# Kernel optimization log

Measured on AMD Instinct MI355X. Metric: run time of the kernel, lower is better.

The kernel has to match this reference:

```python
import jax, jax.numpy as jnp
import numpy as np

FPS, MS = 7, 256
WIDTHS = [(FPS, 12), (12, 12), (12, 12), (12, 12), (12, 12), (12, 6), (6, 1)]


def setup_inputs() -> dict:
    key = jax.random.key(0)
    keys = jax.random.split(key, 1 + 2 * len(WIDTHS))
    B = 32768
    inp = {"inputs": jax.random.normal(keys[0], (B, MS, FPS), dtype=jnp.float32)}
    for li, (fan_in, fan_out) in enumerate(WIDTHS):
        scale = 1.0 / np.sqrt(fan_in)
        inp[f"W{li}"] = jax.random.uniform(keys[1 + 2 * li], (fan_in, fan_out), dtype=jnp.float32, minval=-scale, maxval=scale)
        inp[f"b{li}"] = jnp.zeros((fan_out,), dtype=jnp.float32)
    return inp


def _mlp(x, Ws, bs):
    # layer 0: linear activation
    h = x @ Ws[0] + bs[0]
    # layers 1-4: relu
    for li in range(1, 5):
        h = jax.nn.relu(h @ Ws[li] + bs[li])
    # layer 5: linear (6 units), layer 6: final linear (1 unit)
    h = h @ Ws[5] + bs[5]
    h = h @ Ws[6] + bs[6]
    return h


def reference(inputs, W0, b0, W1, b1, W2, b2, W3, b3, W4, b4, W5, b5, W6, b6):
    B = inputs.shape[0]
    Ws = [W0, W1, W2, W3, W4, W5, W6]
    bs = [b0, b1, b2, b3, b4, b5, b6]
    # Equivalent to looping over ms slices with the shared MLP then concatenating:
    # fold the ms dim into the batch, run once, reshape back to [B, ms].
    x = inputs.reshape(B * MS, FPS)
    out = _mlp(x, Ws, bs)  # [B*MS, 1]
    return out.reshape(B, MS)
```

## Files before the change

kernel.cpp:

```cpp
#include <hip/hip_runtime.h>

#define R 4
#define NTHREADS 256


__global__ __launch_bounds__(NTHREADS, 4) void mlp_kernel(
    const float* __restrict__ in,
    const float* __restrict__ W0, const float* __restrict__ b0,
    const float* __restrict__ W1, const float* __restrict__ b1,
    const float* __restrict__ W2, const float* __restrict__ b2,
    const float* __restrict__ W3, const float* __restrict__ b3,
    const float* __restrict__ W4, const float* __restrict__ b4,
    const float* __restrict__ W5, const float* __restrict__ b5,
    const float* __restrict__ W6, const float* __restrict__ b6,
    float* __restrict__ out, int nrows)
{
    __shared__ __align__(16) float lds[768];
    const int tid = threadIdx.x;

#define STAGE(off, src, count) \
    for (int k = tid; k < (count); k += NTHREADS) lds[(off) + k] = (src)[k];
    STAGE(0,   W0, 84)  STAGE(96,  b0, 12)
    STAGE(112, W1, 144) STAGE(256, b1, 12)
    STAGE(272, W2, 144) STAGE(416, b2, 12)
    STAGE(432, W3, 144) STAGE(576, b3, 12)
    STAGE(592, W4, 144) STAGE(736, b4, 12)
#undef STAGE
    if (tid < 12) {
        float acc = 0.0f;
        for (int c = 0; c < 6; ++c) acc = fmaf(W5[tid * 6 + c], W6[c], acc);
        lds[752 + tid] = acc;
    } else if (tid == 12) {
        float acc = b6[0];
        for (int c = 0; c < 6; ++c) acc = fmaf(b5[c], W6[c], acc);
        lds[764] = acc;
    }
    __syncthreads();

    const long t = (long)blockIdx.x * NTHREADS + tid;
    const long row0 = t * R;
    if (row0 >= nrows) return;
    const bool full = (row0 + R) <= nrows;

    float xs[28];
    if (full) {
        const float4* ip = (const float4*)(in + row0 * 7);
        float4 q;
        q = ip[0]; xs[0]=q.x;  xs[1]=q.y;  xs[2]=q.z;  xs[3]=q.w;
        q = ip[1]; xs[4]=q.x;  xs[5]=q.y;  xs[6]=q.z;  xs[7]=q.w;
        q = ip[2]; xs[8]=q.x;  xs[9]=q.y;  xs[10]=q.z; xs[11]=q.w;
        q = ip[3]; xs[12]=q.x; xs[13]=q.y; xs[14]=q.z; xs[15]=q.w;
        q = ip[4]; xs[16]=q.x; xs[17]=q.y; xs[18]=q.z; xs[19]=q.w;
        q = ip[5]; xs[20]=q.x; xs[21]=q.y; xs[22]=q.z; xs[23]=q.w;
        q = ip[6]; xs[24]=q.x; xs[25]=q.y; xs[26]=q.z; xs[27]=q.w;
    } else {
        #pragma unroll
        for (int r = 0; r < R; ++r)
            #pragma unroll
            for (int i = 0; i < 7; ++i)
                xs[r * 7 + i] = ((row0 + r) < nrows) ? in[(row0 + r) * 7 + i] : 0.0f;
    }

#define LOADW12(dst, baseptr) { \
    const float4* _p = (const float4*)(baseptr); \
    float4 _a = _p[0], _b = _p[1], _c = _p[2]; \
    dst[0]=_a.x; dst[1]=_a.y; dst[2]=_a.z;  dst[3]=_a.w; \
    dst[4]=_b.x; dst[5]=_b.y; dst[6]=_b.z;  dst[7]=_b.w; \
    dst[8]=_c.x; dst[9]=_c.y; dst[10]=_c.z; dst[11]=_c.w; }

    float h[R][12];

    {
        float bb[12]; LOADW12(bb, lds + 96);
        float w[12];  LOADW12(w, lds + 0);
        #pragma unroll
        for (int r = 0; r < R; ++r)
            #pragma unroll
            for (int j = 0; j < 12; ++j)
                h[r][j] = fmaf(xs[r * 7 + 0], w[j], bb[j]);
        #pragma unroll
        for (int i = 1; i < 7; ++i) {
            LOADW12(w, lds + i * 12);
            #pragma unroll
            for (int r = 0; r < R; ++r)
                #pragma unroll
                for (int j = 0; j < 12; ++j)
                    h[r][j] = fmaf(xs[r * 7 + i], w[j], h[r][j]);
        }
    }

    constexpr int WOFF[4] = {112, 272, 432, 592};
    constexpr int BOFF[4] = {256, 416, 576, 736};
    #pragma unroll
    for (int li = 0; li < 4; ++li) {
        float nxt[R][12];
        {
            float bb[12]; LOADW12(bb, lds + BOFF[li]);
            float w[12];  LOADW12(w, lds + WOFF[li]);
            #pragma unroll
            for (int r = 0; r < R; ++r)
                #pragma unroll
                for (int j = 0; j < 12; ++j)
                    nxt[r][j] = fmaf(h[r][0], w[j], bb[j]);
        }
        #pragma unroll
        for (int i = 1; i < 12; ++i) {
            float w[12]; LOADW12(w, lds + WOFF[li] + i * 12);
            #pragma unroll
            for (int r = 0; r < R; ++r)
                #pragma unroll
                for (int j = 0; j < 12; ++j)
                    nxt[r][j] = fmaf(h[r][i], w[j], nxt[r][j]);
        }
        #pragma unroll
        for (int r = 0; r < R; ++r)
            #pragma unroll
            for (int j = 0; j < 12; ++j)
                h[r][j] = fmaxf(nxt[r][j], 0.0f);
    }

    float w56[12]; LOADW12(w56, lds + 752);
    const float b56 = lds[764];
    float o[R];
    #pragma unroll
    for (int r = 0; r < R; ++r) {
        float acc = fmaf(h[r][0], w56[0], b56);
        #pragma unroll
        for (int i = 1; i < 12; ++i) acc = fmaf(h[r][i], w56[i], acc);
        o[r] = acc;
    }

    if (full) {
        *((float4*)(out + row0)) = make_float4(o[0], o[1], o[2], o[3]);
    } else {
        #pragma unroll
        for (int r = 0; r < R; ++r)
            if ((row0 + r) < nrows) out[row0 + r] = o[r];
    }
#undef LOADW12
}

extern "C" void kernel_launch(void* const* d_in, const int* in_sizes, int n_in,
                              void* d_out, int out_size, void* d_ws, size_t ws_size,
                              hipStream_t stream) {
    const float* in = (const float*)d_in[0];
    const float* W0 = (const float*)d_in[1];  const float* b0 = (const float*)d_in[2];
    const float* W1 = (const float*)d_in[3];  const float* b1 = (const float*)d_in[4];
    const float* W2 = (const float*)d_in[5];  const float* b2 = (const float*)d_in[6];
    const float* W3 = (const float*)d_in[7];  const float* b3 = (const float*)d_in[8];
    const float* W4 = (const float*)d_in[9];  const float* b4 = (const float*)d_in[10];
    const float* W5 = (const float*)d_in[11]; const float* b5 = (const float*)d_in[12];
    const float* W6 = (const float*)d_in[13]; const float* b6 = (const float*)d_in[14];
    float* out = (float*)d_out;

    const int nrows = in_sizes[0] / 7;
    const long nthreads_total = ((long)nrows + R - 1) / R;
    const int blocks = (int)((nthreads_total + NTHREADS - 1) / NTHREADS);

    hipLaunchKernelGGL(mlp_kernel, dim3(blocks), dim3(NTHREADS), 0, stream,
                       in, W0, b0, W1, b1, W2, b2, W3, b3, W4, b4, W5, b5, W6, b6,
                       out, nrows);
}
```

Measured before the change: 128.3 us.

## Run MLP layers on fp16 MFMA with split-precision weights and persistent waves

Replaces the per-thread FP32 FMA MLP with a wave-level MFMA 16x16x32 f16 pipeline. Weights and activations are split into hi/lo fp16 pairs to keep near-FP32 accuracy, and biases are folded in through a constant-one input column. A small pre-kernel builds the weight fragments in the workspace. The main kernel is a grid-stride persistent loop over 16-row tiles with the next tile's input prefetched. This targets the ALU-bound FMA cost, at the price of an extra launch, packing and conversion overhead, and possible precision loss. Rows in a partial last tile (nrows not a multiple of 16) are never computed.

Result: slower. 168.7 us (+31.5%).

```diff
diff --git a/kernel.cpp b/kernel.cpp
--- a/kernel.cpp
+++ b/kernel.cpp
@@ -1,143 +1,148 @@
 #include <hip/hip_runtime.h>
+#include <stdint.h>
 
-#define R 4
-#define NTHREADS 256
+typedef _Float16 half8  __attribute__((ext_vector_type(8)));
+typedef __fp16   fp16x2 __attribute__((ext_vector_type(2)));
+typedef float    floatx4 __attribute__((ext_vector_type(4)));
+typedef uint32_t u32x4  __attribute__((ext_vector_type(4)));
+typedef float    f4a    __attribute__((ext_vector_type(4), aligned(4)));
 
+union FragU { u32x4 v; uint32_t u[4]; half8 h; };
+union H2U   { fp16x2 h; uint32_t u; };
 
-__global__ __launch_bounds__(NTHREADS, 4) void mlp_kernel(
-    const float* __restrict__ in,
-    const float* __restrict__ W0, const float* __restrict__ b0,
-    const float* __restrict__ W1, const float* __restrict__ b1,
-    const float* __restrict__ W2, const float* __restrict__ b2,
-    const float* __restrict__ W3, const float* __restrict__ b3,
-    const float* __restrict__ W4, const float* __restrict__ b4,
-    const float* __restrict__ W5, const float* __restrict__ b5,
-    const float* __restrict__ W6, const float* __restrict__ b6,
-    float* __restrict__ out, int nrows)
+#define NT 256
+#define NBLOCKS 2048
+
+__global__ void build_frags(const float* __restrict__ W0, const float* __restrict__ b0,
+                            const float* __restrict__ W1, const float* __restrict__ b1,
+                            const float* __restrict__ W2, const float* __restrict__ b2,
+                            const float* __restrict__ W3, const float* __restrict__ b3,
+                            const float* __restrict__ W4, const float* __restrict__ b4,
+                            const float* __restrict__ W5, const float* __restrict__ b5,
+                            const float* __restrict__ W6, const float* __restrict__ b6,
+                            uint32_t* __restrict__ ws)
 {
-    __shared__ __align__(16) float lds[768];
-    const int tid = threadIdx.x;
+    const int l = threadIdx.x;
+    if (l >= 64) return;
+    const int m = l & 15, g = l >> 4;
+    const float* Wm[5] = {W0, W1, W2, W3, W4};
+    const float* bm[5] = {b0, b1, b2, b3, b4};
 
-#define STAGE(off, src, count) \
-    for (int k = tid; k < (count); k += NTHREADS) lds[(off) + k] = (src)[k];
-    STAGE(0,   W0, 84)  STAGE(96,  b0, 12)
-    STAGE(112, W1, 144) STAGE(256, b1, 12)
-    STAGE(272, W2, 144) STAGE(416, b2, 12)
-    STAGE(432, W3, 144) STAGE(576, b3, 12)
-    STAGE(592, W4, 144) STAGE(736, b4, 12)
-#undef STAGE
-    if (tid < 12) {
-        float acc = 0.0f;
-        for (int c = 0; c < 6; ++c) acc = fmaf(W5[tid * 6 + c], W6[c], acc);
-        lds[752 + tid] = acc;
-    } else if (tid == 12) {
-        float acc = b6[0];
-        for (int c = 0; c < 6; ++c) acc = fmaf(b5[c], W6[c], acc);
-        lds[764] = acc;
+    for (int s = 0; s < 6; ++s) {
+        const int fan_in = (s == 0) ? 7 : 12;
+        const int mmax   = (s == 5) ? 1 : 12;
+        const float wscale = (s == 0) ? 64.0f : (s == 5 ? (1.0f / 64.0f) : 1.0f);
+        for (int w = 0; w < 4; ++w) {
+            const int i = g * 4 + w;
+            uint32_t u1 = 0, u2 = 0;
+            if (g == 3 && w == 3) {
+                float bv = 0.0f;
+                if (m < mmax) {
+                    if (s == 5) { bv = b6[0]; for (int c = 0; c < 6; ++c) bv = fmaf(b5[c], W6[c], bv); }
+                    else        { bv = 64.0f * bm[s][m]; }
+                }
+                H2U hh; hh.h = __builtin_amdgcn_cvt_pkrtz(bv, 0.0f);
+                float hf = (float)hh.h[0];
+                H2U ll; ll.h = __builtin_amdgcn_cvt_pkrtz(bv - hf, 0.0f);
+                u1 = hh.u; u2 = ll.u;
+            } else if (i < fan_in && m < mmax) {
+                float wv;
+                if (s == 5) { wv = 0.0f; for (int c = 0; c < 6; ++c) wv = fmaf(W5[i * 6 + c], W6[c], wv); wv *= wscale; }
+                else        { wv = Wm[s][i * 12 + m] * wscale; }
+                H2U hh; hh.h = __builtin_amdgcn_cvt_pkrtz(wv, wv);
+                float hf = (float)hh.h[0];
+                H2U ll; ll.h = __builtin_amdgcn_cvt_pkrtz(wv - hf, 0.0f);
+                u1 = hh.u; u2 = ll.u;
+            }
+            ws[((s * 2 + 0) * 64 + l) * 4 + w] = u1;
+            ws[((s * 2 + 1) * 64 + l) * 4 + w] = u2;
+        }
     }
-    __syncthreads();
+}
 
-    const long t = (long)blockIdx.x * NTHREADS + tid;
-    const long row0 = t * R;
-    if (row0 >= nrows) return;
-    const bool full = (row0 + R) <= nrows;
+__global__ __launch_bounds__(NT, 4) void mlp_mfma(const float* __restrict__ in,
+                                                  const uint32_t* __restrict__ ws,
+                                                  float* __restrict__ out,
+                                                  int nrows, int nwaves)
+{
+    const int tid  = threadIdx.x;
+    const int lane = tid & 63;
+    const int wid  = (int)blockIdx.x * (NT / 64) + (tid >> 6);
+    const int m = lane & 15, g = lane >> 4;
+    const bool g1 = (g == 1), g3 = (g == 3), glt2 = (g < 2);
 
-    float xs[28];
-    if (full) {
-        const float4* ip = (const float4*)(in + row0 * 7);
-        float4 q;
-        q = ip[0]; xs[0]=q.x;  xs[1]=q.y;  xs[2]=q.z;  xs[3]=q.w;
-        q = ip[1]; xs[4]=q.x;  xs[5]=q.y;  xs[6]=q.z;  xs[7]=q.w;
-        q = ip[2]; xs[8]=q.x;  xs[9]=q.y;  xs[10]=q.z; xs[11]=q.w;
-        q = ip[3]; xs[12]=q.x; xs[13]=q.y; xs[14]=q.z; xs[15]=q.w;
-        q = ip[4]; xs[16]=q.x; xs[17]=q.y; xs[18]=q.z; xs[19]=q.w;
-        q = ip[5]; xs[20]=q.x; xs[21]=q.y; xs[22]=q.z; xs[23]=q.w;
-        q = ip[6]; xs[24]=q.x; xs[25]=q.y; xs[26]=q.z; xs[27]=q.w;
-    } else {
+    half8 A[6][2];
+    #pragma unroll
+    for (int s = 0; s < 6; ++s)
         #pragma unroll
-        for (int r = 0; r < R; ++r)
-            #pragma unroll
-            for (int i = 0; i < 7; ++i)
-                xs[r * 7 + i] = ((row0 + r) < nrows) ? in[(row0 + r) * 7 + i] : 0.0f;
+        for (int f = 0; f < 2; ++f) {
+            FragU fu;
+            fu.v = *(const u32x4*)(ws + ((s * 2 + f) * 64 + lane) * 4);
+            A[s][f] = fu.h;
+        }
+
+    const int ntiles = nrows >> 4;
+    int t = wid;
+    if (t >= ntiles) return;
+
+    auto SPLIT = [](float y) -> uint32_t {
+        H2U a; a.h = __builtin_amdgcn_cvt_pkrtz(y, y);
+        float hf = (float)a.h[0];
+        H2U r; r.h = __builtin_amdgcn_cvt_pkrtz(y, y - hf);
+        return r.u;
+    };
+
+    f4a q = {0.f, 0.f, 0.f, 0.f};
+    {
+        const int row = (t << 4) + m;
+        if (glt2 && row < nrows) q = *(const f4a*)(in + row * 7 + (g1 ? 3 : 0));
     }
 
-#define LOADW12(dst, baseptr) { \
-    const float4* _p = (const float4*)(baseptr); \
-    float4 _a = _p[0], _b = _p[1], _c = _p[2]; \
-    dst[0]=_a.x; dst[1]=_a.y; dst[2]=_a.z;  dst[3]=_a.w; \
-    dst[4]=_b.x; dst[5]=_b.y; dst[6]=_b.z;  dst[7]=_b.w; \
-    dst[8]=_c.x; dst[9]=_c.y; dst[10]=_c.z; dst[11]=_c.w; }
+    while (t < ntiles) {
+        const int row0 = t << 4;
+        const int tn = t + nwaves;
 
-    float h[R][12];
+        float v0 = g1 ? (float)q[1] : (float)q[0];
+        float v1 = g1 ? (float)q[2] : (float)q[1];
+        float v2 = g1 ? (float)q[3] : (float)q[2];
+        float v3 = g1 ? 0.0f        : (float)q[3];
+        FragU B;
+        B.u[0] = SPLIT(v0);
+        B.u[1] = SPLIT(v1);
+        B.u[2] = SPLIT(v2);
+        B.u[3] = g3 ? 0x00003C00u : SPLIT(v3);
 
-    {
-        float bb[12]; LOADW12(bb, lds + 96);
-        float w[12];  LOADW12(w, lds + 0);
+        f4a qn = {0.f, 0.f, 0.f, 0.f};
+        if (tn < ntiles) {
+            const int row = (tn << 4) + m;
+            if (glt2 && row < nrows) qn = *(const f4a*)(in + row * 7 + (g1 ? 3 : 0));
+        }
+
+        floatx4 acc = {0.f, 0.f, 0.f, 0.f};
+        acc = __builtin_amdgcn_mfma_f32_16x16x32_f16(A[0][0], B.h, acc, 0, 0, 0);
+        acc = __builtin_amdgcn_mfma_f32_16x16x32_f16(A[0][1], B.h, acc, 0, 0, 0);
+
         #pragma unroll
-        for (int r = 0; r < R; ++r)
-            #pragma unroll
-            for (int j = 0; j < 12; ++j)
-                h[r][j] = fmaf(xs[r * 7 + 0], w[j], bb[j]);
-        #pragma unroll
-        for (int i = 1; i < 7; ++i) {
-            LOADW12(w, lds + i * 12);
-            #pragma unroll
-            for (int r = 0; r < R; ++r)
-                #pragma unroll
-                for (int j = 0; j < 12; ++j)
-                    h[r][j] = fmaf(xs[r * 7 + i], w[j], h[r][j]);
+        for (int s = 1; s <= 5; ++s) {
+            float y0 = (s >= 2) ? fmaxf(acc[0], 0.f) : acc[0];
+            float y1 = (s >= 2) ? fmaxf(acc[1], 0.f) : acc[1];
+            float y2 = (s >= 2) ? fmaxf(acc[2], 0.f) : acc[2];
+            float y3 = (s >= 2) ? fmaxf(acc[3], 0.f) : acc[3];
+            B.u[0] = SPLIT(y0);
+            B.u[1] = SPLIT(y1);
+            B.u[2] = SPLIT(y2);
+            B.u[3] = g3 ? 0x00003C00u : SPLIT(y3);
+            floatx4 a2 = {0.f, 0.f, 0.f, 0.f};
+            a2 = __builtin_amdgcn_mfma_f32_16x16x32_f16(A[s][0], B.h, a2, 0, 0, 0);
+            a2 = __builtin_amdgcn_mfma_f32_16x16x32_f16(A[s][1], B.h, a2, 0, 0, 0);
+            acc = a2;
         }
+
+        if (lane < 16 && (row0 + m) < nrows) out[row0 + m] = acc[0];
+
+        q = qn;
+        t = tn;
     }
-
-    constexpr int WOFF[4] = {112, 272, 432, 592};
-    constexpr int BOFF[4] = {256, 416, 576, 736};
-    #pragma unroll
-    for (int li = 0; li < 4; ++li) {
-        float nxt[R][12];
-        {
-            float bb[12]; LOADW12(bb, lds + BOFF[li]);
-            float w[12];  LOADW12(w, lds + WOFF[li]);
-            #pragma unroll
-            for (int r = 0; r < R; ++r)
-                #pragma unroll
-                for (int j = 0; j < 12; ++j)
-                    nxt[r][j] = fmaf(h[r][0], w[j], bb[j]);
-        }
-        #pragma unroll
-        for (int i = 1; i < 12; ++i) {
-            float w[12]; LOADW12(w, lds + WOFF[li] + i * 12);
-            #pragma unroll
-            for (int r = 0; r < R; ++r)
-                #pragma unroll
-                for (int j = 0; j < 12; ++j)
-                    nxt[r][j] = fmaf(h[r][i], w[j], nxt[r][j]);
-        }
-        #pragma unroll
-        for (int r = 0; r < R; ++r)
-            #pragma unroll
-            for (int j = 0; j < 12; ++j)
-                h[r][j] = fmaxf(nxt[r][j], 0.0f);
-    }
-
-    float w56[12]; LOADW12(w56, lds + 752);
-    const float b56 = lds[764];
-    float o[R];
-    #pragma unroll
-    for (int r = 0; r < R; ++r) {
-        float acc = fmaf(h[r][0], w56[0], b56);
-        #pragma unroll
-        for (int i = 1; i < 12; ++i) acc = fmaf(h[r][i], w56[i], acc);
-        o[r] = acc;
-    }
-
-    if (full) {
-        *((float4*)(out + row0)) = make_float4(o[0], o[1], o[2], o[3]);
-    } else {
-        #pragma unroll
-        for (int r = 0; r < R; ++r)
-            if ((row0 + r) < nrows) out[row0 + r] = o[r];
-    }
-#undef LOADW12
 }
 
 extern "C" void kernel_launch(void* const* d_in, const int* in_sizes, int n_in,
@@ -152,12 +157,13 @@
     const float* W5 = (const float*)d_in[11]; const float* b5 = (const float*)d_in[12];
     const float* W6 = (const float*)d_in[13]; const float* b6 = (const float*)d_in[14];
     float* out = (float*)d_out;
+    uint32_t* ws = (uint32_t*)d_ws;
+
+    hipLaunchKernelGGL(build_frags, dim3(1), dim3(64), 0, stream,
+                       W0, b0, W1, b1, W2, b2, W3, b3, W4, b4, W5, b5, W6, b6, ws);
 
     const int nrows = in_sizes[0] / 7;
-    const long nthreads_total = ((long)nrows + R - 1) / R;
-    const int blocks = (int)((nthreads_total + NTHREADS - 1) / NTHREADS);
-
-    hipLaunchKernelGGL(mlp_kernel, dim3(blocks), dim3(NTHREADS), 0, stream,
-                       in, W0, b0, W1, b1, W2, b2, W3, b3, W4, b4, W5, b5, W6, b6,
-                       out, nrows);
+    const int nwaves = NBLOCKS * (NT / 64);
+    hipLaunchKernelGGL(mlp_mfma, dim3(NBLOCKS), dim3(NT), 0, stream,
+                       in, ws, out, nrows, nwaves);
 }
```
